# Kernel tuning notes

Measured on AMD Instinct MI355X. Metric: run time of the kernel, lower is better.

The kernel has to match this reference:

```python
import jax, jax.numpy as jnp
import numpy as np

N, L, D, F, NUM_BAGS = 262144, 1024, 128, 32, 256


def setup_inputs() -> dict:
    key = jax.random.key(0)
    ks = jax.random.split(key, 12)
    x = jax.random.normal(ks[0], (N, L), dtype=jnp.float32)
    idxs = jnp.sort(jax.random.randint(ks[1], (N,), 0, NUM_BAGS, dtype=jnp.int64))
    def lin(k, fan_in, fan_out):
        s = 1.0 / np.sqrt(fan_in)
        return jax.random.uniform(k, (fan_in, fan_out), jnp.float32, -s, s)
    W1 = lin(ks[2], L, D);  b1 = jnp.zeros((D,), jnp.float32)
    Wt = lin(ks[3], D, F);  bt = jnp.zeros((F,), jnp.float32)
    Ws = lin(ks[4], D, F);  bs = jnp.zeros((F,), jnp.float32)
    Wa = lin(ks[5], F, 1);  ba = jnp.zeros((1,), jnp.float32)
    Wp = lin(ks[6], D, F);  bp = jnp.zeros((F,), jnp.float32)
    return {"x": x, "idxs": idxs, "W1": W1, "b1": b1, "Wt": Wt, "bt": bt,
            "Ws": Ws, "bs": bs, "Wa": Wa, "ba": ba, "Wp": Wp, "bp": bp}


def reference(x, idxs, W1, b1, Wt, bt, Ws, bs, Wa, ba, Wp, bp):
    # feature extractor (Dropout is identity at eval time)
    H = jax.nn.relu(x @ W1 + b1)                       # [N, D]
    # gated attention scores
    At = jnp.tanh(H @ Wt + bt)                         # [N, F]
    As = jax.nn.sigmoid(H @ Ws + bs)                   # [N, F]
    a = ((At * As) @ Wa + ba)[:, 0]                    # [N]
    # per-bag (segment) softmax, numerically stable
    amax = jax.ops.segment_max(a, idxs, num_segments=NUM_BAGS)   # [B]
    w = jnp.exp(a - amax[idxs])                         # [N]
    den = jax.ops.segment_sum(w, idxs, num_segments=NUM_BAGS)    # [B]
    w = w / den[idxs]
    # segment weighted reduce: M[b] = sum_i w_i * H_i over bag b
    M = jax.ops.segment_sum(w[:, None] * H, idxs, num_segments=NUM_BAGS)  # [B, D]
    # projector + L2 normalize (torch F.normalize eps=1e-12)
    proj = M @ Wp + bp                                  # [B, F]
    nrm = jnp.maximum(jnp.linalg.norm(proj, axis=1, keepdims=True), 1e-12)
    proj = proj / nrm
    return M, proj
```

## Files before the change

kernel.cpp:

```cpp
#include <hip/hip_runtime.h>
#include <hip/hip_bf16.h>

#define NTOT 262144
#define LDIM 1024
#define DDIM 128
#define FDIM 32
#define NBAGS 256

typedef __attribute__((ext_vector_type(8))) short bf16x8;
typedef __attribute__((ext_vector_type(4))) float f32x4;

__device__ __forceinline__ unsigned short f2b(float f) {
    __hip_bfloat16 h = __float2bfloat16(f);
    return __builtin_bit_cast(unsigned short, h);
}
__device__ __forceinline__ float b2f(unsigned short u) {
    union { float f; unsigned int i; } c;
    c.i = ((unsigned int)u) << 16;
    return c.f;
}

__global__ void k_prep(const float* __restrict__ W1, const float* __restrict__ Wt,
                       const float* __restrict__ Ws,
                       ushort* __restrict__ w1t2, ushort* __restrict__ wtT,
                       ushort* __restrict__ wsT,
                       float* __restrict__ Mraw, float* __restrict__ dden) {
    int gid = blockIdx.x * 256 + threadIdx.x;
    if (gid < LDIM * DDIM) {
        int col = gid & 127, k = gid >> 7;
        int kt = k >> 6, ko = k & 63;
        int cc = ko >> 3, kr = ko & 7;
        w1t2[kt * 8192 + col * 64 + (cc ^ (col & 7)) * 8 + kr] = f2b(W1[gid]);
    }
    if (gid < DDIM * FDIM) {
        int f = gid & 31, d = gid >> 5;
        wtT[f * 128 + d] = f2b(Wt[gid]);
        wsT[f * 128 + d] = f2b(Ws[gid]);
    }
    if (gid < NBAGS * DDIM) Mraw[gid] = 0.0f;
    if (gid < NBAGS) dden[gid] = 0.0f;
}

__global__ __launch_bounds__(512, 4) void k_fused_gemm(
    const float* __restrict__ x, const ushort* __restrict__ w1t2,
    const ushort* __restrict__ wtT, const ushort* __restrict__ wsT,
    const float* __restrict__ b1,
    const float* __restrict__ bt, const float* __restrict__ bs,
    const float* __restrict__ Wa, const float* __restrict__ ba,
    const int* __restrict__ idxs,
    float* __restrict__ Mraw, float* __restrict__ dden)
{
    __shared__ __align__(16) ushort sA2[2][8192];
    __shared__ __align__(16) ushort sB2[2][8192];
    __shared__ float sb1[128];
    __shared__ float sbt[32], sbs[32], sWa[32];
    __shared__ float sw[128];
    __shared__ int   sbag[128];

    const int t    = threadIdx.x;
    const int lane = t & 63;
    const int wave = t >> 6;
    const int wr   = wave >> 1, wc = wave & 1;
    const int lq   = lane >> 4, lr = lane & 15;
    const int row0 = blockIdx.x * 128;

    if (t < 128) { sb1[t] = b1[t]; sbag[t] = idxs[row0 + t]; }
    if (t < 32)  { sbt[t] = bt[t]; sbs[t] = bs[t]; sWa[t] = Wa[t]; }
    const float ba0 = ba[0];

    f32x4 acc[2][4];
#pragma unroll
    for (int m = 0; m < 2; ++m)
#pragma unroll
        for (int n = 0; n < 4; ++n) acc[m][n] = 0;

    const int arow  = t >> 4;
    const int acol4 = (t & 15) * 4;
    const float* xb = x + (size_t)(row0 + arow) * LDIM + acol4;
    const int a_base = (((acol4 >> 3) ^ (arow & 7)) << 4) + (acol4 & 7) * 2;
    const ushort* bb = w1t2 + t * 8;

    float4 av[4];
    bf16x8 bv[2];
#pragma unroll
    for (int j = 0; j < 4; ++j) av[j] = *(const float4*)(xb + j * (32 * LDIM));
#pragma unroll
    for (int jj = 0; jj < 2; ++jj) bv[jj] = *(const bf16x8*)(bb + jj * 4096);

    for (int kt = 0; kt < 16; ++kt) {
        const int p = kt & 1;
        char* sA = (char*)sA2[p];
        char* sB = (char*)sB2[p];

#pragma unroll
        for (int j = 0; j < 4; ++j) {
            float4 f = av[j];
            uint2 pk;
            pk.x = (unsigned)f2b(f.x) | ((unsigned)f2b(f.y) << 16);
            pk.y = (unsigned)f2b(f.z) | ((unsigned)f2b(f.w) << 16);
            *(uint2*)(sA + (arow + 32 * j) * 128 + a_base) = pk;
        }
#pragma unroll
        for (int jj = 0; jj < 2; ++jj)
            *(bf16x8*)(sB + t * 16 + jj * 8192) = bv[jj];

        __syncthreads();

        if (kt < 15) {
            const float* xk = xb + (kt + 1) * 64;
#pragma unroll
            for (int j = 0; j < 4; ++j) av[j] = *(const float4*)(xk + j * (32 * LDIM));
            const ushort* bk = bb + (kt + 1) * 8192;
#pragma unroll
            for (int jj = 0; jj < 2; ++jj) bv[jj] = *(const bf16x8*)(bk + jj * 4096);
        }

#pragma unroll
        for (int kk = 0; kk < 2; ++kk) {
            bf16x8 aF[2], bF[4];
#pragma unroll
            for (int m = 0; m < 2; ++m) {
                int ra = wr * 32 + m * 16 + lr;
                aF[m] = *(const bf16x8*)(sA + ra * 128 + (((kk * 4 + lq) ^ (ra & 7)) << 4));
            }
#pragma unroll
            for (int n = 0; n < 4; ++n) {
                int cb = wc * 64 + n * 16 + lr;
                bF[n] = *(const bf16x8*)(sB + cb * 128 + (((kk * 4 + lq) ^ (cb & 7)) << 4));
            }
#pragma unroll
            for (int m = 0; m < 2; ++m)
#pragma unroll
                for (int n = 0; n < 4; ++n)
                    acc[m][n] = __builtin_amdgcn_mfma_f32_16x16x32_bf16(aF[m], bF[n], acc[m][n], 0, 0, 0);
        }
    }
    __syncthreads();

    char* sH = (char*)sA2;
#pragma unroll
    for (int m = 0; m < 2; ++m) {
#pragma unroll
        for (int n = 0; n < 4; ++n) {
            const int colg = wc * 64 + n * 16 + lr;
            const float bias = sb1[colg];
#pragma unroll
            for (int r = 0; r < 4; ++r) {
                const int rowl = wr * 32 + m * 16 + lq * 4 + r;
                float h = acc[m][n][r] + bias;
                h = fmaxf(h, 0.0f);
                *(ushort*)(sH + rowl * 256 + (((colg >> 3) ^ (rowl & 15)) << 4) + (colg & 7) * 2) = f2b(h);
            }
        }
    }
    __syncthreads();

    {
        f32x4 at_[2], as_[2];
#pragma unroll
        for (int n = 0; n < 2; ++n) { at_[n] = 0; as_[n] = 0; }

#pragma unroll
        for (int kk = 0; kk < 4; ++kk) {
            bf16x8 aH, bT[2], bS[2];
            const int slot = kk * 4 + lq;
            const int ra = wave * 16 + lr;
            aH = *(const bf16x8*)(sH + ra * 256 + ((slot ^ (ra & 15)) << 4));
#pragma unroll
            for (int n = 0; n < 2; ++n) {
                const int f = n * 16 + lr;
                bT[n] = *(const bf16x8*)(wtT + f * 128 + kk * 32 + lq * 8);
                bS[n] = *(const bf16x8*)(wsT + f * 128 + kk * 32 + lq * 8);
            }
#pragma unroll
            for (int n = 0; n < 2; ++n) {
                at_[n] = __builtin_amdgcn_mfma_f32_16x16x32_bf16(aH, bT[n], at_[n], 0, 0, 0);
                as_[n] = __builtin_amdgcn_mfma_f32_16x16x32_bf16(aH, bS[n], as_[n], 0, 0, 0);
            }
        }

#pragma unroll
        for (int r = 0; r < 4; ++r) {
            float s = 0.f;
#pragma unroll
            for (int n = 0; n < 2; ++n) {
                const int f = n * 16 + lr;
                float tv = tanhf(at_[n][r] + sbt[f]);
                float sg = 1.0f / (1.0f + __expf(-(as_[n][r] + sbs[f])));
                s += tv * sg * sWa[f];
            }
            s += __shfl_xor(s, 1);
            s += __shfl_xor(s, 2);
            s += __shfl_xor(s, 4);
            s += __shfl_xor(s, 8);
            if (lr == 0)
                sw[wave * 16 + lq * 4 + r] = __expf(s + ba0);
        }
    }
    __syncthreads();

    {
        const int d = t & 127, q = t >> 7;
        const int r0 = q * 32;
        float accv = 0.f, accw = 0.f;
        int curbag = sbag[r0];
        for (int r = 0; r < 32; ++r) {
            const int rr = r0 + r;
            const int bg = sbag[rr];
            if (bg != curbag) {
                atomicAdd(&Mraw[curbag * 128 + d], accv);
                if (d == 0) atomicAdd(&dden[curbag], accw);
                accv = 0.f; accw = 0.f; curbag = bg;
            }
            const float w = sw[rr];
            const ushort hv = *(const ushort*)(sH + rr * 256 + ((((d >> 3) ^ (rr & 15))) << 4) + (d & 7) * 2);
            accv += w * b2f(hv);
            accw += w;
        }
        atomicAdd(&Mraw[curbag * 128 + d], accv);
        if (d == 0) atomicAdd(&dden[curbag], accw);
    }
}

__global__ __launch_bounds__(128) void k_final(
    const float* __restrict__ Mraw, const float* __restrict__ dden,
    const float* __restrict__ Wp, const float* __restrict__ bp,
    float* __restrict__ out)
{
    __shared__ float sM[128];
    const int b = blockIdx.x, t = threadIdx.x;
    const float den = dden[b];
    const float inv_den = den > 0.f ? 1.0f / den : 0.0f;

    float m = Mraw[b * 128 + t] * inv_den;
    sM[t] = m;
    out[b * 128 + t] = m;
    __syncthreads();

    if (t < 32) {
        float p = bp[t];
        for (int d = 0; d < 128; ++d) p += sM[d] * Wp[d * 32 + t];
        float ss = p * p;
#pragma unroll
        for (int mm = 1; mm < 32; mm <<= 1) ss += __shfl_xor(ss, mm);
        float nrm = sqrtf(ss);
        out[32768 + b * 32 + t] = p / fmaxf(nrm, 1e-12f);
    }
}

extern "C" void kernel_launch(void* const* d_in, const int* in_sizes, int n_in,
                              void* d_out, int out_size, void* d_ws, size_t ws_size,
                              hipStream_t stream)
{
    const float* x  = (const float*)d_in[0];
    const int*   idxs = (const int*)d_in[1];
    const float* W1 = (const float*)d_in[2];
    const float* b1 = (const float*)d_in[3];
    const float* Wt = (const float*)d_in[4];
    const float* bt = (const float*)d_in[5];
    const float* Ws = (const float*)d_in[6];
    const float* bs = (const float*)d_in[7];
    const float* Wa = (const float*)d_in[8];
    const float* ba = (const float*)d_in[9];
    const float* Wp = (const float*)d_in[10];
    const float* bp = (const float*)d_in[11];
    float* out = (float*)d_out;

    char* ws = (char*)d_ws;
    float*  Mraw = (float*)ws;
    float*  dden = (float*)(ws + 131072);
    ushort* w1t2 = (ushort*)(ws + 132096);
    ushort* wtT  = (ushort*)(ws + 132096 + 262144);
    ushort* wsT  = (ushort*)(ws + 132096 + 262144 + 8192);

    k_prep<<<512, 256, 0, stream>>>(W1, Wt, Ws, w1t2, wtT, wsT, Mraw, dden);
    k_fused_gemm<<<2048, 512, 0, stream>>>(x, w1t2, wtT, wsT, b1, bt, bs, Wa, ba, idxs, Mraw, dden);
    k_final<<<NBAGS, 128, 0, stream>>>(Mraw, dden, Wp, bp, out);
}
```

Before: 256.4 us.

## Switch to register double-buffered prefetch two tiles ahead with single-buffered LDS

The K loop now prefetches global tiles two iterations ahead into two register buffers and uses a single LDS buffer, adding a barrier before each LDS write. This deepens global-load latency hiding and halves LDS use, which could allow more resident blocks. In exchange it raises register pressure under launch_bounds(512,4), adds a barrier per iteration, and no longer overlaps LDS writes with the previous tile's MFMA reads.

Result: faster. 235.2 us (-8.3%).

```diff
diff --git a/kernel.cpp b/kernel.cpp
--- a/kernel.cpp
+++ b/kernel.cpp
@@ -50,8 +50,7 @@
     const int* __restrict__ idxs,
     float* __restrict__ Mraw, float* __restrict__ dden)
 {
-    __shared__ __align__(16) ushort sA2[2][8192];
-    __shared__ __align__(16) ushort sB2[2][8192];
+    __shared__ __align__(16) ushort sAB[16384];
     __shared__ float sb1[128];
     __shared__ float sbt[32], sbs[32], sWa[32];
     __shared__ float sw[128];
@@ -74,27 +73,34 @@
 #pragma unroll
         for (int n = 0; n < 4; ++n) acc[m][n] = 0;
 
+    char* sA = (char*)sAB;
+    char* sB = (char*)sAB + 16384;
+
     const int arow  = t >> 4;
     const int acol4 = (t & 15) * 4;
     const float* xb = x + (size_t)(row0 + arow) * LDIM + acol4;
     const int a_base = (((acol4 >> 3) ^ (arow & 7)) << 4) + (acol4 & 7) * 2;
     const ushort* bb = w1t2 + t * 8;
 
-    float4 av[4];
-    bf16x8 bv[2];
-#pragma unroll
-    for (int j = 0; j < 4; ++j) av[j] = *(const float4*)(xb + j * (32 * LDIM));
-#pragma unroll
-    for (int jj = 0; jj < 2; ++jj) bv[jj] = *(const bf16x8*)(bb + jj * 4096);
+    float4 av[2][4];
+    bf16x8 bv[2][2];
+#pragma unroll
+    for (int j = 0; j < 4; ++j) av[0][j] = *(const float4*)(xb + j * (32 * LDIM));
+#pragma unroll
+    for (int jj = 0; jj < 2; ++jj) bv[0][jj] = *(const bf16x8*)(bb + jj * 4096);
+#pragma unroll
+    for (int j = 0; j < 4; ++j) av[1][j] = *(const float4*)(xb + 64 + j * (32 * LDIM));
+#pragma unroll
+    for (int jj = 0; jj < 2; ++jj) bv[1][jj] = *(const bf16x8*)(bb + 8192 + jj * 4096);
 
     for (int kt = 0; kt < 16; ++kt) {
         const int p = kt & 1;
-        char* sA = (char*)sA2[p];
-        char* sB = (char*)sB2[p];
+
+        __syncthreads();
 
 #pragma unroll
         for (int j = 0; j < 4; ++j) {
-            float4 f = av[j];
+            float4 f = av[p][j];
             uint2 pk;
             pk.x = (unsigned)f2b(f.x) | ((unsigned)f2b(f.y) << 16);
             pk.y = (unsigned)f2b(f.z) | ((unsigned)f2b(f.w) << 16);
@@ -102,17 +108,17 @@
         }
 #pragma unroll
         for (int jj = 0; jj < 2; ++jj)
-            *(bf16x8*)(sB + t * 16 + jj * 8192) = bv[jj];
+            *(bf16x8*)(sB + t * 16 + jj * 8192) = bv[p][jj];
 
         __syncthreads();
 
-        if (kt < 15) {
-            const float* xk = xb + (kt + 1) * 64;
-#pragma unroll
-            for (int j = 0; j < 4; ++j) av[j] = *(const float4*)(xk + j * (32 * LDIM));
-            const ushort* bk = bb + (kt + 1) * 8192;
-#pragma unroll
-            for (int jj = 0; jj < 2; ++jj) bv[jj] = *(const bf16x8*)(bk + jj * 4096);
+        if (kt < 14) {
+            const float* xk = xb + (kt + 2) * 64;
+#pragma unroll
+            for (int j = 0; j < 4; ++j) av[p][j] = *(const float4*)(xk + j * (32 * LDIM));
+            const ushort* bk = bb + (kt + 2) * 8192;
+#pragma unroll
+            for (int jj = 0; jj < 2; ++jj) bv[p][jj] = *(const bf16x8*)(bk + jj * 4096);
         }
 
 #pragma unroll
@@ -137,7 +143,7 @@
     }
     __syncthreads();
 
-    char* sH = (char*)sA2;
+    char* sH = (char*)sAB;
 #pragma unroll
     for (int m = 0; m < 2; ++m) {
 #pragma unroll
```

## Load MFMA operands directly from global memory, bypassing LDS staging

Applied to the files above, without the earlier changes.

The main GEMM loop no longer stages x and W1 tiles through double-buffered shared memory with barriers. Each wave now loads its A fragments (fp32 x, converted to bf16 in registers) and B fragments (a plain transposed bf16 W1 layout) straight from global memory into MFMA operand registers. This removes the LDS writes, the LDS reads and the per-iteration __syncthreads. In exchange, each element is loaded redundantly by several waves, the global accesses are strided rather than coalesced, and the fully unrolled loop raises register pressure.

Result: slower. 546.5 us (+113.1%).

```diff
diff --git a/kernel.cpp b/kernel.cpp
--- a/kernel.cpp
+++ b/kernel.cpp
@@ -22,15 +22,13 @@
 
 __global__ void k_prep(const float* __restrict__ W1, const float* __restrict__ Wt,
                        const float* __restrict__ Ws,
-                       ushort* __restrict__ w1t2, ushort* __restrict__ wtT,
+                       ushort* __restrict__ w1t, ushort* __restrict__ wtT,
                        ushort* __restrict__ wsT,
                        float* __restrict__ Mraw, float* __restrict__ dden) {
     int gid = blockIdx.x * 256 + threadIdx.x;
     if (gid < LDIM * DDIM) {
         int col = gid & 127, k = gid >> 7;
-        int kt = k >> 6, ko = k & 63;
-        int cc = ko >> 3, kr = ko & 7;
-        w1t2[kt * 8192 + col * 64 + (cc ^ (col & 7)) * 8 + kr] = f2b(W1[gid]);
+        w1t[col * 1024 + k] = f2b(W1[gid]);
     }
     if (gid < DDIM * FDIM) {
         int f = gid & 31, d = gid >> 5;
@@ -42,7 +40,7 @@
 }
 
 __global__ __launch_bounds__(512, 4) void k_fused_gemm(
-    const float* __restrict__ x, const ushort* __restrict__ w1t2,
+    const float* __restrict__ x, const ushort* __restrict__ w1t,
     const ushort* __restrict__ wtT, const ushort* __restrict__ wsT,
     const float* __restrict__ b1,
     const float* __restrict__ bt, const float* __restrict__ bs,
@@ -50,8 +48,7 @@
     const int* __restrict__ idxs,
     float* __restrict__ Mraw, float* __restrict__ dden)
 {
-    __shared__ __align__(16) ushort sA2[2][8192];
-    __shared__ __align__(16) ushort sB2[2][8192];
+    __shared__ __align__(16) ushort sHbuf[16384];
     __shared__ float sb1[128];
     __shared__ float sbt[32], sbs[32], sWa[32];
     __shared__ float sw[128];
@@ -74,70 +71,52 @@
 #pragma unroll
         for (int n = 0; n < 4; ++n) acc[m][n] = 0;
 
-    const int arow  = t >> 4;
-    const int acol4 = (t & 15) * 4;
-    const float* xb = x + (size_t)(row0 + arow) * LDIM + acol4;
-    const int a_base = (((acol4 >> 3) ^ (arow & 7)) << 4) + (acol4 & 7) * 2;
-    const ushort* bb = w1t2 + t * 8;
-
-    float4 av[4];
-    bf16x8 bv[2];
-#pragma unroll
-    for (int j = 0; j < 4; ++j) av[j] = *(const float4*)(xb + j * (32 * LDIM));
-#pragma unroll
-    for (int jj = 0; jj < 2; ++jj) bv[jj] = *(const bf16x8*)(bb + jj * 4096);
-
+    const float* xpA0 = x + (size_t)(row0 + wr * 32 + lr) * LDIM + lq * 8;
+    const float* xpA1 = xpA0 + 16 * LDIM;
+    const ushort* wbB = w1t + (size_t)(wc * 64 + lr) * 1024 + lq * 8;
+
+#pragma unroll
     for (int kt = 0; kt < 16; ++kt) {
-        const int p = kt & 1;
-        char* sA = (char*)sA2[p];
-        char* sB = (char*)sB2[p];
-
-#pragma unroll
-        for (int j = 0; j < 4; ++j) {
-            float4 f = av[j];
-            uint2 pk;
-            pk.x = (unsigned)f2b(f.x) | ((unsigned)f2b(f.y) << 16);
-            pk.y = (unsigned)f2b(f.z) | ((unsigned)f2b(f.w) << 16);
-            *(uint2*)(sA + (arow + 32 * j) * 128 + a_base) = pk;
-        }
-#pragma unroll
-        for (int jj = 0; jj < 2; ++jj)
-            *(bf16x8*)(sB + t * 16 + jj * 8192) = bv[jj];
-
-        __syncthreads();
-
-        if (kt < 15) {
-            const float* xk = xb + (kt + 1) * 64;
-#pragma unroll
-            for (int j = 0; j < 4; ++j) av[j] = *(const float4*)(xk + j * (32 * LDIM));
-            const ushort* bk = bb + (kt + 1) * 8192;
-#pragma unroll
-            for (int jj = 0; jj < 2; ++jj) bv[jj] = *(const bf16x8*)(bk + jj * 4096);
-        }
+        const int ko = kt * 64;
+        float4 ax[2][2][2];
+        bf16x8 bx[2][4];
+
+#pragma unroll
+        for (int kk = 0; kk < 2; ++kk)
+#pragma unroll
+            for (int h = 0; h < 2; ++h) {
+                ax[0][kk][h] = *(const float4*)(xpA0 + ko + kk * 32 + h * 4);
+                ax[1][kk][h] = *(const float4*)(xpA1 + ko + kk * 32 + h * 4);
+            }
+#pragma unroll
+        for (int kk = 0; kk < 2; ++kk)
+#pragma unroll
+            for (int n = 0; n < 4; ++n)
+                bx[kk][n] = *(const bf16x8*)(wbB + n * 16384 + ko + kk * 32);
 
 #pragma unroll
         for (int kk = 0; kk < 2; ++kk) {
-            bf16x8 aF[2], bF[4];
+            bf16x8 aF[2];
 #pragma unroll
             for (int m = 0; m < 2; ++m) {
-                int ra = wr * 32 + m * 16 + lr;
-                aF[m] = *(const bf16x8*)(sA + ra * 128 + (((kk * 4 + lq) ^ (ra & 7)) << 4));
-            }
-#pragma unroll
-            for (int n = 0; n < 4; ++n) {
-                int cb = wc * 64 + n * 16 + lr;
-                bF[n] = *(const bf16x8*)(sB + cb * 128 + (((kk * 4 + lq) ^ (cb & 7)) << 4));
+                union { bf16x8 v; ushort u[8]; } pk;
+                float4 f0 = ax[m][kk][0], f1 = ax[m][kk][1];
+                pk.u[0] = f2b(f0.x); pk.u[1] = f2b(f0.y);
+                pk.u[2] = f2b(f0.z); pk.u[3] = f2b(f0.w);
+                pk.u[4] = f2b(f1.x); pk.u[5] = f2b(f1.y);
+                pk.u[6] = f2b(f1.z); pk.u[7] = f2b(f1.w);
+                aF[m] = pk.v;
             }
 #pragma unroll
             for (int m = 0; m < 2; ++m)
 #pragma unroll
                 for (int n = 0; n < 4; ++n)
-                    acc[m][n] = __builtin_amdgcn_mfma_f32_16x16x32_bf16(aF[m], bF[n], acc[m][n], 0, 0, 0);
-        }
-    }
-    __syncthreads();
-
-    char* sH = (char*)sA2;
+                    acc[m][n] = __builtin_amdgcn_mfma_f32_16x16x32_bf16(aF[m], bx[kk][n], acc[m][n], 0, 0, 0);
+        }
+    }
+    __syncthreads();
+
+    char* sH = (char*)sHbuf;
 #pragma unroll
     for (int m = 0; m < 2; ++m) {
 #pragma unroll
@@ -269,11 +248,11 @@
     char* ws = (char*)d_ws;
     float*  Mraw = (float*)ws;
     float*  dden = (float*)(ws + 131072);
-    ushort* w1t2 = (ushort*)(ws + 132096);
+    ushort* w1t  = (ushort*)(ws + 132096);
     ushort* wtT  = (ushort*)(ws + 132096 + 262144);
     ushort* wsT  = (ushort*)(ws + 132096 + 262144 + 8192);
 
-    k_prep<<<512, 256, 0, stream>>>(W1, Wt, Ws, w1t2, wtT, wsT, Mraw, dden);
-    k_fused_gemm<<<2048, 512, 0, stream>>>(x, w1t2, wtT, wsT, b1, bt, bs, Wa, ba, idxs, Mraw, dden);
+    k_prep<<<512, 256, 0, stream>>>(W1, Wt, Ws, w1t, wtT, wsT, Mraw, dden);
+    k_fused_gemm<<<2048, 512, 0, stream>>>(x, w1t, wtT, wsT, b1, bt, bs, Wa, ba, idxs, Mraw, dden);
     k_final<<<NBAGS, 128, 0, stream>>>(Mraw, dden, Wp, bp, out);
 }
```
